# Kernel tuning notes

Hardware: AMD Instinct MI355X
Metric: run time of the kernel (lower is better)

The kernel has to match this reference:

```python
import jax, jax.numpy as jnp
import numpy as np
import math

D = 256; NH = 8; NL = 1; K = 5; P = K * K; HD = D // NH; DFF = 1024
N = 8192; H = 512; W = 512


def _kernel_indices():
    # odd kernel: linspace(-(K-1)/2, (K-1)/2, K) / K, meshgrid ij, stacked (x=j, y=i)
    idx = jnp.linspace(-(K - 1) / 2, (K - 1) / 2, K)
    i, j = jnp.meshgrid(idx, idx, indexing='ij')
    return jnp.stack([j, i], axis=-1).reshape(-1, 2) / K  # (P, 2)


def _ln(x, g, b, eps=1e-5):
    m = x.mean(-1, keepdims=True)
    v = ((x - m) ** 2).mean(-1, keepdims=True)
    return (x - m) / jnp.sqrt(v + eps) * g + b


def setup_inputs() -> dict:
    key = jax.random.key(0)
    ks = jax.random.split(key, 20)
    s = 0.02
    inp = {
        'query': jax.random.normal(ks[0], (1, N, D), jnp.float32),
        'memory': jax.random.normal(ks[1], (1, H * W, D), jnp.float32),
        'ref_windows': jax.random.uniform(ks[2], (1, N, 8), jnp.float32),
        'memory_shape': jnp.array([[H, W]], jnp.int32),
        'memory_start_idx': jnp.zeros((1,), jnp.int64),
        # pos embed MLP(8 -> D -> D -> D)
        'Wp1': jax.random.normal(ks[3], (D, 8)) * s, 'bp1': jnp.zeros((D,)),
        'Wp2': jax.random.normal(ks[4], (D, D)) * s, 'bp2': jnp.zeros((D,)),
        'Wp3': jax.random.normal(ks[5], (D, D)) * s, 'bp3': jnp.zeros((D,)),
        # Box3dAttention
        'Wv': jax.random.normal(ks[6], (D, D)) * s, 'bv': jnp.zeros((D,)),
        'Wa': jax.random.normal(ks[7], (NH * NL * P, D)) * s, 'ba': jnp.zeros((NH * NL * P,)),
        'Wb': jax.random.normal(ks[8], (NH * NL * 5, D)) * s, 'bb': jnp.zeros((NH * NL * 5,)),
        'Wo': jax.random.normal(ks[9], (D, D)) * s, 'bo': jnp.zeros((D,)),
        # FFN + norms
        'W1': jax.random.normal(ks[10], (DFF, D)) * s, 'b1': jnp.zeros((DFF,)),
        'W2': jax.random.normal(ks[11], (D, DFF)) * s, 'b2': jnp.zeros((D,)),
        'g2': jnp.ones((D,)), 'be2': jnp.zeros((D,)),
        'g3': jnp.ones((D,)), 'be3': jnp.zeros((D,)),
    }
    return inp


def reference(query, memory, ref_windows, memory_shape, memory_start_idx,
              Wp1, bp1, Wp2, bp2, Wp3, bp3, Wv, bv, Wa, ba, Wb, bb, Wo, bo,
              W1, b1, W2, b2, g2, be2, g3, be3):
    B, n, _ = query.shape  # B == 1, single level (NL == 1)
    # query positional embedding from ref windows (3-layer MLP)
    qp = jax.nn.relu(ref_windows @ Wp1.T + bp1)
    qp = jax.nn.relu(qp @ Wp2.T + bp2)
    qp = qp @ Wp3.T + bp3
    q = query + qp

    # --- Box3dAttention ---
    v = (memory @ Wv.T + bv).reshape(B, H * W, NH, HD)
    attn = jax.nn.softmax((q @ Wa.T + ba).reshape(B, n, NH, NL * P), axis=-1)
    attn = attn.reshape(B, n, NH, NL, P)

    off = (q @ Wb.T + bb).reshape(B, n, NH, NL, 5)
    off_box, off_ang = off[..., :4], off[..., 4:]
    rw = ref_windows[:, :, None, None]                     # (B,n,1,1,8)
    ref_boxes = rw[..., jnp.array([0, 1, 3, 4])]           # cx,cy,w,l
    ref_angle = rw[..., 6:7]
    angles = (ref_angle + off_ang / 16.0) * (2.0 * math.pi)  # (B,n,NH,NL,1)
    boxes = ref_boxes + off_box / 8.0 * ref_boxes[..., jnp.array([2, 3, 2, 3])]
    center = boxes[..., None, :2]                          # (B,n,NH,NL,1,2)
    size = jax.nn.relu(boxes[..., None, 2:])
    grid = _kernel_indices() * size                        # (B,n,NH,NL,P,2)
    c, sgn = jnp.cos(angles), jnp.sin(angles)
    rot = jnp.stack([c, -sgn, sgn, c], -1).reshape(B, n, NH, NL, 1, 2, 2)
    loc = center + (grid[..., None, :] * rot).sum(-1)      # (B,n,NH,NL,P,2) in [0,1]

    # bilinear sampling (grid_sample, align_corners=False, zero padding), single level
    loc0 = loc[0, :, :, 0]                                 # (n,NH,P,2)
    vh = v[0].transpose(1, 0, 2)                           # (NH,HW,HD)
    x = loc0[..., 0] * W - 0.5
    y = loc0[..., 1] * H - 0.5
    x0 = jnp.floor(x); y0 = jnp.floor(y)
    hidx = jnp.arange(NH)[None, :, None]
    out = jnp.zeros((n, NH, P, HD), v.dtype)
    for dx, dy in ((0, 0), (1, 0), (0, 1), (1, 1)):
        xi = x0 + dx; yi = y0 + dy
        wgt = (1.0 - jnp.abs(x - xi)) * (1.0 - jnp.abs(y - yi))
        valid = (xi >= 0) & (xi <= W - 1) & (yi >= 0) & (yi <= H - 1)
        idx = (jnp.clip(yi, 0, H - 1) * W + jnp.clip(xi, 0, W - 1)).astype(jnp.int32)
        g = vh[hidx, idx]                                  # (n,NH,P,HD)
        out = out + jnp.where(valid, wgt, 0.0)[..., None] * g
    out = (out * attn[0, :, :, 0, :, None]).sum(2)         # (n,NH,HD)
    q2 = out.reshape(1, n, D) @ Wo.T + bo

    # residual + LN + FFN + LN
    xq = _ln(query + q2, g2, be2)
    ff = jax.nn.relu(xq @ W1.T + b1) @ W2.T + b2
    return _ln(xq + ff, g3, be3)
```

## Files before the change

kernel.cpp:

```cpp
#include <hip/hip_runtime.h>
#include <hip/hip_bf16.h>
#include <math.h>

#define NQ 8192
#define DD 256
#define NHD 8
#define HDD 32
#define PP 25
#define HH 512
#define WW 512
#define HWSZ (HH * WW)
#define DFF 1024

typedef __bf16 bf16_t;
typedef bf16_t bf16x8 __attribute__((ext_vector_type(8)));
typedef bf16_t bf16x4 __attribute__((ext_vector_type(4)));
typedef float f32x4 __attribute__((ext_vector_type(4)));

__global__ __launch_bounds__(256, 2) void wv_kernel(
    const float* __restrict__ A, const bf16_t* __restrict__ Wt,
    const float* __restrict__ bias, __hip_bfloat16* __restrict__ V) {
  const int tid = threadIdx.x;
  const int wave = tid >> 6;
  const int lane = tid & 63;
  const int l15 = lane & 15;
  const int quad = lane >> 4;
  const int wslice = wave * 64;
  const int base = blockIdx.x * 256;

  bf16x8 bfr[4][8];
#pragma unroll
  for (int j = 0; j < 4; j++) {
    const bf16_t* wp = Wt + (size_t)(wslice + j * 16 + l15) * 256 + quad * 8;
#pragma unroll
    for (int kt = 0; kt < 8; kt++) bfr[j][kt] = *(const bf16x8*)(wp + kt * 32);
  }
  float bsv[4];
#pragma unroll
  for (int j = 0; j < 4; j++) bsv[j] = bias[wslice + j * 16 + l15];

  for (int c = 0; c < 16; c++) {
    const int m0 = base + c * 16;
    const float* ap = A + (size_t)(m0 + l15) * 256 + quad * 8;
    float4 av[8][2];
#pragma unroll
    for (int kt = 0; kt < 8; kt++) {
      av[kt][0] = *(const float4*)(ap + kt * 32);
      av[kt][1] = *(const float4*)(ap + kt * 32 + 4);
    }
    f32x4 acc[4];
#pragma unroll
    for (int j = 0; j < 4; j++) acc[j] = (f32x4){0.f, 0.f, 0.f, 0.f};
#pragma unroll
    for (int kt = 0; kt < 8; kt++) {
      bf16x8 afr;
      afr[0] = (bf16_t)av[kt][0].x;
      afr[1] = (bf16_t)av[kt][0].y;
      afr[2] = (bf16_t)av[kt][0].z;
      afr[3] = (bf16_t)av[kt][0].w;
      afr[4] = (bf16_t)av[kt][1].x;
      afr[5] = (bf16_t)av[kt][1].y;
      afr[6] = (bf16_t)av[kt][1].z;
      afr[7] = (bf16_t)av[kt][1].w;
#pragma unroll
      for (int j = 0; j < 4; j++)
        acc[j] = __builtin_amdgcn_mfma_f32_16x16x32_bf16(afr, bfr[j][kt],
                                                         acc[j], 0, 0, 0);
    }
#pragma unroll
    for (int j = 0; j < 4; j++) {
      const int col = wslice + j * 16 + l15;
#pragma unroll
      for (int r = 0; r < 4; r++) {
        const int row = m0 + quad * 4 + r;
        V[(size_t)row * DD + col] = __float2bfloat16(acc[j][r] + bsv[j]);
      }
    }
  }
}

template <int RELU, int ADD_RES, int BF16_OUT>
__global__ __launch_bounds__(256) void gemm_mfma(
    const bf16_t* __restrict__ A, const bf16_t* __restrict__ Wt,
    const float* __restrict__ bias, const float* __restrict__ res,
    void* __restrict__ Cout, int M, int N, int K) {
  __shared__ bf16_t As[128][32];
  __shared__ bf16_t Bs[128][32];
  const int tid = threadIdx.x;
  const int bn = blockIdx.x * 128;
  const int bm = blockIdx.y * 128;
  const int wave = tid >> 6;
  const int lane = tid & 63;
  const int l15 = lane & 15;
  const int quad = lane >> 4;
  const int wm = (wave & 1) * 64;
  const int wn = (wave >> 1) * 64;

  f32x4 acc[4][4];
#pragma unroll
  for (int i = 0; i < 4; i++)
#pragma unroll
    for (int j = 0; j < 4; j++) acc[i][j] = (f32x4){0.f, 0.f, 0.f, 0.f};

  const int srow = tid >> 2;
  const int skq = (tid & 3) * 8;

  for (int k0 = 0; k0 < K; k0 += 32) {
#pragma unroll
    for (int c = 0; c < 2; c++) {
      const int row = c * 64 + srow;
      const bf16_t* gp = A + (long)(bm + row) * K + k0 + skq;
      bf16_t* lp = &As[0][0] + (c * 2048 + wave * 512);
      __builtin_amdgcn_global_load_lds(
          (const __attribute__((address_space(1))) void*)gp,
          (__attribute__((address_space(3))) void*)lp, 16, 0, 0);
    }
#pragma unroll
    for (int c = 0; c < 2; c++) {
      const int row = c * 64 + srow;
      int wrow = bn + row;
      if (wrow >= N) wrow = N - 1;
      const bf16_t* gp = Wt + (long)wrow * K + k0 + skq;
      bf16_t* lp = &Bs[0][0] + (c * 2048 + wave * 512);
      __builtin_amdgcn_global_load_lds(
          (const __attribute__((address_space(1))) void*)gp,
          (__attribute__((address_space(3))) void*)lp, 16, 0, 0);
    }
    __syncthreads();
    bf16x8 af[4], bfr[4];
#pragma unroll
    for (int i = 0; i < 4; i++)
      af[i] = *(bf16x8*)&As[wm + i * 16 + l15][quad * 8];
#pragma unroll
    for (int j = 0; j < 4; j++)
      bfr[j] = *(bf16x8*)&Bs[wn + j * 16 + l15][quad * 8];
#pragma unroll
    for (int i = 0; i < 4; i++)
#pragma unroll
      for (int j = 0; j < 4; j++)
        acc[i][j] = __builtin_amdgcn_mfma_f32_16x16x32_bf16(af[i], bfr[j],
                                                            acc[i][j], 0, 0, 0);
    __syncthreads();
  }

  float bsv[4];
#pragma unroll
  for (int j = 0; j < 4; j++) {
    const int n = bn + wn + j * 16 + l15;
    bsv[j] = (n < N) ? bias[n] : 0.f;
  }
#pragma unroll
  for (int i = 0; i < 4; i++) {
#pragma unroll
    for (int r = 0; r < 4; r++) {
      const int m = bm + wm + i * 16 + quad * 4 + r;
#pragma unroll
      for (int j = 0; j < 4; j++) {
        const int n = bn + wn + j * 16 + l15;
        if (n < N) {
          float v = acc[i][j][r] + bsv[j];
          if (ADD_RES) v += res[(long)m * N + n];
          if (RELU) v = fmaxf(v, 0.f);
          if (BF16_OUT)
            ((__hip_bfloat16*)Cout)[(long)m * N + n] = __float2bfloat16(v);
          else
            ((float*)Cout)[(long)m * N + n] = v;
        }
      }
    }
  }
}

struct CastArgs {
  const float* src[8];
  __hip_bfloat16* dst[8];
  int len[8];
};
__global__ __launch_bounds__(256) void cast_weights(CastArgs a) {
  const int seg = blockIdx.y;
  const int base = blockIdx.x * 1024 + threadIdx.x * 4;
  if (base >= a.len[seg]) return;
  const float4 v = *(const float4*)(a.src[seg] + base);
  __hip_bfloat16* d = a.dst[seg] + base;
  d[0] = __float2bfloat16(v.x);
  d[1] = __float2bfloat16(v.y);
  d[2] = __float2bfloat16(v.z);
  d[3] = __float2bfloat16(v.w);
}

__global__ __launch_bounds__(256) void qp1_kernel(
    const float* __restrict__ rw, const float* __restrict__ Wp1,
    const float* __restrict__ bp1, __hip_bfloat16* __restrict__ out) {
  const int m = blockIdx.x;
  const int d = threadIdx.x;
  __shared__ float r[8];
  if (d < 8) r[d] = rw[m * 8 + d];
  __syncthreads();
  float s = bp1[d];
#pragma unroll
  for (int j = 0; j < 8; j++) s += r[j] * Wp1[d * 8 + j];
  out[(long)m * DD + d] = __float2bfloat16(fmaxf(s, 0.f));
}

__global__ __launch_bounds__(256) void attn_loc_kernel(
    const float* __restrict__ logits, const float* __restrict__ offp,
    const float* __restrict__ rw, float* __restrict__ attn,
    float* __restrict__ loc) {
  const int m = blockIdx.x;
  const int t = threadIdx.x;
  __shared__ float sl[200];
  __shared__ float soff[40];
  __shared__ float srw[8];
  if (t < 200) sl[t] = logits[(long)m * 200 + t];
  if (t >= 208 && t < 248) soff[t - 208] = offp[(long)m * 40 + (t - 208)];
  if (t >= 200 && t < 208) srw[t - 200] = rw[(long)m * 8 + (t - 200)];
  __syncthreads();
  if (t < 8) {
    float mx = -1e30f;
    for (int p = 0; p < 25; p++) mx = fmaxf(mx, sl[t * 25 + p]);
    float s = 0.f;
    for (int p = 0; p < 25; p++) s += __expf(sl[t * 25 + p] - mx);
    const float inv = 1.f / s;
    for (int p = 0; p < 25; p++)
      attn[(long)m * 200 + t * 25 + p] = __expf(sl[t * 25 + p] - mx) * inv;
  }
  if (t < 200) {
    const int h = t / 25;
    const int p = t - h * 25;
    const float cx = srw[0], cy = srw[1], w0 = srw[3], h0 = srw[4],
                ra = srw[6];
    const float ob0 = soff[h * 5 + 0], ob1 = soff[h * 5 + 1],
                ob2 = soff[h * 5 + 2], ob3 = soff[h * 5 + 3],
                oa = soff[h * 5 + 4];
    const float ang = (ra + oa * (1.f / 16.f)) * 6.28318530717958647692f;
    const float bx = cx + ob0 * 0.125f * w0;
    const float by = cy + ob1 * 0.125f * h0;
    const float bw = fmaxf(w0 + ob2 * 0.125f * w0, 0.f);
    const float bh = fmaxf(h0 + ob3 * 0.125f * h0, 0.f);
    const float gx = (float)((p % 5) - 2) * 0.2f * bw;
    const float gy = (float)((p / 5) - 2) * 0.2f * bh;
    float sn, cs;
    __sincosf(ang, &sn, &cs);
    loc[((long)m * 200 + t) * 2 + 0] = bx + cs * gx - sn * gy;
    loc[((long)m * 200 + t) * 2 + 1] = by + sn * gx + cs * gy;
  }
}

__global__ __launch_bounds__(256) void sample_kernel(
    const bf16_t* __restrict__ v, const float* __restrict__ attn,
    const float* __restrict__ loc, bf16_t* __restrict__ out) {
  const int m = blockIdx.x;
  const int t = threadIdx.x;
  const int h = t >> 5;
  const int sub = t & 31;
  const int tap = sub >> 3;
  const int ch4 = (sub & 7) * 4;
  const float fdx = (float)(tap & 1);
  const float fdy = (float)(tap >> 1);
  __shared__ float sat[200];
  __shared__ float slc[400];
  if (t < 200) sat[t] = attn[(long)m * 200 + t];
  slc[t] = loc[(long)m * 400 + t];
  if (t < 144) slc[256 + t] = loc[(long)m * 400 + 256 + t];
  __syncthreads();
  float a0 = 0.f, a1 = 0.f, a2 = 0.f, a3 = 0.f;
  const bf16_t* vb = v + h * HDD + ch4;
  for (int p = 0; p < 25; p++) {
    const float lx = slc[(h * 25 + p) * 2 + 0];
    const float ly = slc[(h * 25 + p) * 2 + 1];
    const float aw = sat[h * 25 + p];
    const float x = lx * (float)WW - 0.5f;
    const float y = ly * (float)HH - 0.5f;
    const float x0 = floorf(x);
    const float y0 = floorf(y);
    const float xi = x0 + fdx;
    const float yi = y0 + fdy;
    const float wgt = (1.f - fabsf(x - xi)) * (1.f - fabsf(y - yi));
    const bool valid = (xi >= 0.f) && (xi <= (float)(WW - 1)) &&
                       (yi >= 0.f) && (yi <= (float)(HH - 1));
    const int xc = (int)fminf(fmaxf(xi, 0.f), (float)(WW - 1));
    const int yc = (int)fminf(fmaxf(yi, 0.f), (float)(HH - 1));
    const int idx = yc * WW + xc;
    const bf16x4 g = *(const bf16x4*)(vb + (size_t)idx * DD);
    const float wv = valid ? aw * wgt : 0.f;
    a0 += wv * (float)g[0];
    a1 += wv * (float)g[1];
    a2 += wv * (float)g[2];
    a3 += wv * (float)g[3];
  }
  a0 += __shfl_xor(a0, 8);  a1 += __shfl_xor(a1, 8);
  a2 += __shfl_xor(a2, 8);  a3 += __shfl_xor(a3, 8);
  a0 += __shfl_xor(a0, 16); a1 += __shfl_xor(a1, 16);
  a2 += __shfl_xor(a2, 16); a3 += __shfl_xor(a3, 16);
  if (tap == 0) {
    bf16x4 o;
    o[0] = (bf16_t)a0; o[1] = (bf16_t)a1; o[2] = (bf16_t)a2; o[3] = (bf16_t)a3;
    *(bf16x4*)(out + (size_t)m * DD + h * HDD + ch4) = o;
  }
}

__global__ __launch_bounds__(256) void ln_kernel(
    const float* __restrict__ x, const float* __restrict__ resid,
    const float* __restrict__ g, const float* __restrict__ b,
    float* __restrict__ out, __hip_bfloat16* __restrict__ out_bf) {
  const int m = blockIdx.x;
  const int d = threadIdx.x;
  const float v = x[(long)m * DD + d] + resid[(long)m * DD + d];
  __shared__ float red[256];
  __shared__ float mean_s, inv_s;
  red[d] = v;
  __syncthreads();
  for (int s = 128; s > 0; s >>= 1) {
    if (d < s) red[d] += red[d + s];
    __syncthreads();
  }
  if (d == 0) mean_s = red[0] * (1.f / 256.f);
  __syncthreads();
  const float mu = mean_s;
  const float diff = v - mu;
  red[d] = diff * diff;
  __syncthreads();
  for (int s = 128; s > 0; s >>= 1) {
    if (d < s) red[d] += red[d + s];
    __syncthreads();
  }
  if (d == 0) inv_s = rsqrtf(red[0] * (1.f / 256.f) + 1e-5f);
  __syncthreads();
  const float o = diff * inv_s * g[d] + b[d];
  out[(long)m * DD + d] = o;
  if (out_bf) out_bf[(long)m * DD + d] = __float2bfloat16(o);
}

extern "C" void kernel_launch(void* const* d_in, const int* in_sizes, int n_in,
                              void* d_out, int out_size, void* d_ws,
                              size_t ws_size, hipStream_t stream) {
  const float* query = (const float*)d_in[0];
  const float* memory = (const float*)d_in[1];
  const float* rw = (const float*)d_in[2];
  const float* Wp1 = (const float*)d_in[5];
  const float* bp1 = (const float*)d_in[6];
  const float* Wp2 = (const float*)d_in[7];
  const float* bp2 = (const float*)d_in[8];
  const float* Wp3 = (const float*)d_in[9];
  const float* bp3 = (const float*)d_in[10];
  const float* Wv = (const float*)d_in[11];
  const float* bv = (const float*)d_in[12];
  const float* Wa = (const float*)d_in[13];
  const float* ba = (const float*)d_in[14];
  const float* Wb = (const float*)d_in[15];
  const float* bb = (const float*)d_in[16];
  const float* Wo = (const float*)d_in[17];
  const float* bo = (const float*)d_in[18];
  const float* W1 = (const float*)d_in[19];
  const float* b1 = (const float*)d_in[20];
  const float* W2 = (const float*)d_in[21];
  const float* b2 = (const float*)d_in[22];
  const float* g2 = (const float*)d_in[23];
  const float* be2 = (const float*)d_in[24];
  const float* g3 = (const float*)d_in[25];
  const float* be3 = (const float*)d_in[26];

  char* ws = (char*)d_ws;
  size_t off = 0;
  auto alloc = [&](size_t bytes) {
    void* p = ws + off;
    off += (bytes + 255) & ~(size_t)255;
    return p;
  };
  __hip_bfloat16* vbuf = (__hip_bfloat16*)alloc((size_t)HWSZ * DD * 2);
  __hip_bfloat16* qp1bf = (__hip_bfloat16*)alloc((size_t)NQ * DD * 2);
  __hip_bfloat16* qp2bf = (__hip_bfloat16*)alloc((size_t)NQ * DD * 2);
  __hip_bfloat16* qbf = (__hip_bfloat16*)alloc((size_t)NQ * DD * 2);
  __hip_bfloat16* oabf = (__hip_bfloat16*)alloc((size_t)NQ * DD * 2);
  __hip_bfloat16* xqbf = (__hip_bfloat16*)alloc((size_t)NQ * DD * 2);
  __hip_bfloat16* h1bf = (__hip_bfloat16*)alloc((size_t)NQ * DFF * 2);
  float* xq32 = (float*)alloc((size_t)NQ * DD * 4);
  float* f32buf = (float*)alloc((size_t)NQ * DD * 4);
  float* offbuf = (float*)alloc((size_t)NQ * 40 * 4);
  float* attnbuf = (float*)alloc((size_t)NQ * 200 * 4);
  float* locbuf = (float*)alloc((size_t)NQ * 200 * 2 * 4);
  __hip_bfloat16* Wp2b = (__hip_bfloat16*)alloc(65536 * 2);
  __hip_bfloat16* Wp3b = (__hip_bfloat16*)alloc(65536 * 2);
  __hip_bfloat16* Wvb = (__hip_bfloat16*)alloc(65536 * 2);
  __hip_bfloat16* Wab = (__hip_bfloat16*)alloc(51200 * 2);
  __hip_bfloat16* Wbb = (__hip_bfloat16*)alloc(10240 * 2);
  __hip_bfloat16* Wob = (__hip_bfloat16*)alloc(65536 * 2);
  __hip_bfloat16* W1b = (__hip_bfloat16*)alloc(262144 * 2);
  __hip_bfloat16* W2b = (__hip_bfloat16*)alloc(262144 * 2);
  (void)ws_size;

  CastArgs ca;
  ca.src[0] = Wp2; ca.dst[0] = Wp2b; ca.len[0] = 65536;
  ca.src[1] = Wp3; ca.dst[1] = Wp3b; ca.len[1] = 65536;
  ca.src[2] = Wv;  ca.dst[2] = Wvb;  ca.len[2] = 65536;
  ca.src[3] = Wa;  ca.dst[3] = Wab;  ca.len[3] = 51200;
  ca.src[4] = Wb;  ca.dst[4] = Wbb;  ca.len[4] = 10240;
  ca.src[5] = Wo;  ca.dst[5] = Wob;  ca.len[5] = 65536;
  ca.src[6] = W1;  ca.dst[6] = W1b;  ca.len[6] = 262144;
  ca.src[7] = W2;  ca.dst[7] = W2b;  ca.len[7] = 262144;
  cast_weights<<<dim3(256, 8), 256, 0, stream>>>(ca);

  qp1_kernel<<<NQ, 256, 0, stream>>>(rw, Wp1, bp1, qp1bf);
  gemm_mfma<1, 0, 1><<<dim3(2, NQ / 128), 256, 0, stream>>>(
      (const bf16_t*)qp1bf, (const bf16_t*)Wp2b, bp2, nullptr, qp2bf, NQ, DD,
      DD);
  gemm_mfma<0, 1, 1><<<dim3(2, NQ / 128), 256, 0, stream>>>(
      (const bf16_t*)qp2bf, (const bf16_t*)Wp3b, bp3, query, qbf, NQ, DD, DD);
  wv_kernel<<<HWSZ / 256, 256, 0, stream>>>(memory, (const bf16_t*)Wvb, bv,
                                            vbuf);
  gemm_mfma<0, 0, 0><<<dim3(2, NQ / 128), 256, 0, stream>>>(
      (const bf16_t*)qbf, (const bf16_t*)Wab, ba, nullptr, f32buf, NQ, 200,
      DD);
  gemm_mfma<0, 0, 0><<<dim3(1, NQ / 128), 256, 0, stream>>>(
      (const bf16_t*)qbf, (const bf16_t*)Wbb, bb, nullptr, offbuf, NQ, 40, DD);
  attn_loc_kernel<<<NQ, 256, 0, stream>>>(f32buf, offbuf, rw, attnbuf, locbuf);
  sample_kernel<<<NQ, 256, 0, stream>>>((const bf16_t*)vbuf, attnbuf, locbuf,
                                        (bf16_t*)oabf);
  gemm_mfma<0, 0, 0><<<dim3(2, NQ / 128), 256, 0, stream>>>(
      (const bf16_t*)oabf, (const bf16_t*)Wob, bo, nullptr, f32buf, NQ, DD,
      DD);
  ln_kernel<<<NQ, 256, 0, stream>>>(f32buf, query, g2, be2, xq32, xqbf);
  gemm_mfma<1, 0, 1><<<dim3(8, NQ / 128), 256, 0, stream>>>(
      (const bf16_t*)xqbf, (const bf16_t*)W1b, b1, nullptr, h1bf, NQ, DFF, DD);
  gemm_mfma<0, 0, 0><<<dim3(2, NQ / 128), 256, 0, stream>>>(
      (const bf16_t*)h1bf, (const bf16_t*)W2b, b2, nullptr, f32buf, NQ, DD,
      DFF);
  ln_kernel<<<NQ, 256, 0, stream>>>(f32buf, xq32, g3, be3, (float*)d_out,
                                    nullptr);
}
```

Measured before the change: 825.6 us.

## Retile memory value projection, merge attn/offset GEMMs, fuse softmax+loc into sampler

The value projection over the 262144-row memory is retiled. Each block now stages a 64-column slice of the weights in shared memory, computes a 256x64 output tile with 4x4 MFMA accumulators per wave, and writes bf16x4 vector stores instead of scalar ones. The attention-logit and box-offset GEMMs are merged into one 240-column GEMM by using a split bias. The softmax and sampling-location computation moves into the sampling kernel, which removes a kernel launch and the attn/loc buffer round trips. In exchange, each block in the value projection rereads the fp32 memory rows four times, once per column slice, and the sampling kernel gains an extra barrier.

```diff
diff --git a/kernel.cpp b/kernel.cpp
--- a/kernel.cpp
+++ b/kernel.cpp
@@ -17,64 +17,72 @@
 typedef bf16_t bf16x4 __attribute__((ext_vector_type(4)));
 typedef float f32x4 __attribute__((ext_vector_type(4)));
 
-__global__ __launch_bounds__(256, 2) void wv_kernel(
+__global__ __launch_bounds__(256) void wv_kernel(
     const float* __restrict__ A, const bf16_t* __restrict__ Wt,
-    const float* __restrict__ bias, __hip_bfloat16* __restrict__ V) {
+    const float* __restrict__ bias, bf16_t* __restrict__ V) {
+  __shared__ bf16_t Bs[64][264];
   const int tid = threadIdx.x;
   const int wave = tid >> 6;
   const int lane = tid & 63;
   const int l15 = lane & 15;
   const int quad = lane >> 4;
-  const int wslice = wave * 64;
-  const int base = blockIdx.x * 256;
-
-  bf16x8 bfr[4][8];
-#pragma unroll
-  for (int j = 0; j < 4; j++) {
-    const bf16_t* wp = Wt + (size_t)(wslice + j * 16 + l15) * 256 + quad * 8;
-#pragma unroll
-    for (int kt = 0; kt < 8; kt++) bfr[j][kt] = *(const bf16x8*)(wp + kt * 32);
-  }
+  const int nbase = (blockIdx.x & 3) * 64;
+  const int mbase = (blockIdx.x >> 2) * 256;
+
+  {
+    const int rr = tid & 63;
+    const int seg = tid >> 6;
+    const int wrow = nbase + ((rr & 15) * 4 + (rr >> 4));
+    const bf16_t* gp = Wt + (size_t)wrow * 256 + seg * 64;
+#pragma unroll
+    for (int u = 0; u < 8; u++)
+      *(bf16x8*)&Bs[rr][seg * 64 + u * 8] = *(const bf16x8*)(gp + u * 8);
+  }
+  __syncthreads();
+
+  const int m0 = mbase + wave * 64;
+  f32x4 acc[4][4];
+#pragma unroll
+  for (int i = 0; i < 4; i++)
+#pragma unroll
+    for (int j = 0; j < 4; j++) acc[i][j] = (f32x4){0.f, 0.f, 0.f, 0.f};
   float bsv[4];
 #pragma unroll
-  for (int j = 0; j < 4; j++) bsv[j] = bias[wslice + j * 16 + l15];
-
-  for (int c = 0; c < 16; c++) {
-    const int m0 = base + c * 16;
-    const float* ap = A + (size_t)(m0 + l15) * 256 + quad * 8;
-    float4 av[8][2];
-#pragma unroll
-    for (int kt = 0; kt < 8; kt++) {
-      av[kt][0] = *(const float4*)(ap + kt * 32);
-      av[kt][1] = *(const float4*)(ap + kt * 32 + 4);
-    }
-    f32x4 acc[4];
-#pragma unroll
-    for (int j = 0; j < 4; j++) acc[j] = (f32x4){0.f, 0.f, 0.f, 0.f};
-#pragma unroll
-    for (int kt = 0; kt < 8; kt++) {
-      bf16x8 afr;
-      afr[0] = (bf16_t)av[kt][0].x;
-      afr[1] = (bf16_t)av[kt][0].y;
-      afr[2] = (bf16_t)av[kt][0].z;
-      afr[3] = (bf16_t)av[kt][0].w;
-      afr[4] = (bf16_t)av[kt][1].x;
-      afr[5] = (bf16_t)av[kt][1].y;
-      afr[6] = (bf16_t)av[kt][1].z;
-      afr[7] = (bf16_t)av[kt][1].w;
-#pragma unroll
-      for (int j = 0; j < 4; j++)
-        acc[j] = __builtin_amdgcn_mfma_f32_16x16x32_bf16(afr, bfr[j][kt],
-                                                         acc[j], 0, 0, 0);
+  for (int j = 0; j < 4; j++) bsv[j] = bias[nbase + l15 * 4 + j];
+
+#pragma unroll
+  for (int kt = 0; kt < 8; kt++) {
+    const int k0 = kt * 32;
+    bf16x8 afr[4];
+#pragma unroll
+    for (int i = 0; i < 4; i++) {
+      const float* ap = A + (size_t)(m0 + i * 16 + l15) * 256 + k0 + quad * 8;
+      const float4 a0 = *(const float4*)ap;
+      const float4 a1 = *(const float4*)(ap + 4);
+      afr[i][0] = (bf16_t)a0.x; afr[i][1] = (bf16_t)a0.y;
+      afr[i][2] = (bf16_t)a0.z; afr[i][3] = (bf16_t)a0.w;
+      afr[i][4] = (bf16_t)a1.x; afr[i][5] = (bf16_t)a1.y;
+      afr[i][6] = (bf16_t)a1.z; afr[i][7] = (bf16_t)a1.w;
     }
 #pragma unroll
     for (int j = 0; j < 4; j++) {
-      const int col = wslice + j * 16 + l15;
-#pragma unroll
-      for (int r = 0; r < 4; r++) {
-        const int row = m0 + quad * 4 + r;
-        V[(size_t)row * DD + col] = __float2bfloat16(acc[j][r] + bsv[j]);
-      }
+      const bf16x8 bfr = *(const bf16x8*)&Bs[j * 16 + l15][k0 + quad * 8];
+#pragma unroll
+      for (int i = 0; i < 4; i++)
+        acc[i][j] = __builtin_amdgcn_mfma_f32_16x16x32_bf16(afr[i], bfr,
+                                                            acc[i][j], 0, 0, 0);
+    }
+  }
+
+#pragma unroll
+  for (int i = 0; i < 4; i++) {
+#pragma unroll
+    for (int r = 0; r < 4; r++) {
+      const int row = m0 + i * 16 + quad * 4 + r;
+      bf16x4 o;
+#pragma unroll
+      for (int j = 0; j < 4; j++) o[j] = (bf16_t)(acc[i][j][r] + bsv[j]);
+      *(bf16x4*)(V + (size_t)row * DD + nbase + l15 * 4) = o;
     }
   }
 }
@@ -82,8 +90,9 @@
 template <int RELU, int ADD_RES, int BF16_OUT>
 __global__ __launch_bounds__(256) void gemm_mfma(
     const bf16_t* __restrict__ A, const bf16_t* __restrict__ Wt,
-    const float* __restrict__ bias, const float* __restrict__ res,
-    void* __restrict__ Cout, int M, int N, int K) {
+    const float* __restrict__ bias, const float* __restrict__ bias2, int split,
+    const float* __restrict__ res, void* __restrict__ Cout, int M, int N,
+    int K) {
   __shared__ bf16_t As[128][32];
   __shared__ bf16_t Bs[128][32];
   const int tid = threadIdx.x;
@@ -147,7 +156,7 @@
 #pragma unroll
   for (int j = 0; j < 4; j++) {
     const int n = bn + wn + j * 16 + l15;
-    bsv[j] = (n < N) ? bias[n] : 0.f;
+    bsv[j] = (n >= N) ? 0.f : (n < split ? bias[n] : bias2[n - split]);
   }
 #pragma unroll
   for (int i = 0; i < 4; i++) {
@@ -202,53 +211,9 @@
   out[(long)m * DD + d] = __float2bfloat16(fmaxf(s, 0.f));
 }
 
-__global__ __launch_bounds__(256) void attn_loc_kernel(
-    const float* __restrict__ logits, const float* __restrict__ offp,
-    const float* __restrict__ rw, float* __restrict__ attn,
-    float* __restrict__ loc) {
-  const int m = blockIdx.x;
-  const int t = threadIdx.x;
-  __shared__ float sl[200];
-  __shared__ float soff[40];
-  __shared__ float srw[8];
-  if (t < 200) sl[t] = logits[(long)m * 200 + t];
-  if (t >= 208 && t < 248) soff[t - 208] = offp[(long)m * 40 + (t - 208)];
-  if (t >= 200 && t < 208) srw[t - 200] = rw[(long)m * 8 + (t - 200)];
-  __syncthreads();
-  if (t < 8) {
-    float mx = -1e30f;
-    for (int p = 0; p < 25; p++) mx = fmaxf(mx, sl[t * 25 + p]);
-    float s = 0.f;
-    for (int p = 0; p < 25; p++) s += __expf(sl[t * 25 + p] - mx);
-    const float inv = 1.f / s;
-    for (int p = 0; p < 25; p++)
-      attn[(long)m * 200 + t * 25 + p] = __expf(sl[t * 25 + p] - mx) * inv;
-  }
-  if (t < 200) {
-    const int h = t / 25;
-    const int p = t - h * 25;
-    const float cx = srw[0], cy = srw[1], w0 = srw[3], h0 = srw[4],
-                ra = srw[6];
-    const float ob0 = soff[h * 5 + 0], ob1 = soff[h * 5 + 1],
-                ob2 = soff[h * 5 + 2], ob3 = soff[h * 5 + 3],
-                oa = soff[h * 5 + 4];
-    const float ang = (ra + oa * (1.f / 16.f)) * 6.28318530717958647692f;
-    const float bx = cx + ob0 * 0.125f * w0;
-    const float by = cy + ob1 * 0.125f * h0;
-    const float bw = fmaxf(w0 + ob2 * 0.125f * w0, 0.f);
-    const float bh = fmaxf(h0 + ob3 * 0.125f * h0, 0.f);
-    const float gx = (float)((p % 5) - 2) * 0.2f * bw;
-    const float gy = (float)((p / 5) - 2) * 0.2f * bh;
-    float sn, cs;
-    __sincosf(ang, &sn, &cs);
-    loc[((long)m * 200 + t) * 2 + 0] = bx + cs * gx - sn * gy;
-    loc[((long)m * 200 + t) * 2 + 1] = by + sn * gx + cs * gy;
-  }
-}
-
 __global__ __launch_bounds__(256) void sample_kernel(
-    const bf16_t* __restrict__ v, const float* __restrict__ attn,
-    const float* __restrict__ loc, bf16_t* __restrict__ out) {
+    const bf16_t* __restrict__ v, const float* __restrict__ lg,
+    const float* __restrict__ rw, bf16_t* __restrict__ out) {
   const int m = blockIdx.x;
   const int t = threadIdx.x;
   const int h = t >> 5;
@@ -257,11 +222,40 @@
   const int ch4 = (sub & 7) * 4;
   const float fdx = (float)(tap & 1);
   const float fdy = (float)(tap >> 1);
+  __shared__ float sl[240];
+  __shared__ float srw[8];
   __shared__ float sat[200];
   __shared__ float slc[400];
-  if (t < 200) sat[t] = attn[(long)m * 200 + t];
-  slc[t] = loc[(long)m * 400 + t];
-  if (t < 144) slc[256 + t] = loc[(long)m * 400 + 256 + t];
+  if (t < 240) sl[t] = lg[(long)m * 240 + t];
+  if (t >= 240 && t < 248) srw[t - 240] = rw[(long)m * 8 + (t - 240)];
+  __syncthreads();
+  if (t < 8) {
+    float mx = -1e30f;
+    for (int p = 0; p < 25; p++) mx = fmaxf(mx, sl[t * 25 + p]);
+    float s = 0.f;
+    for (int p = 0; p < 25; p++) s += __expf(sl[t * 25 + p] - mx);
+    const float inv = 1.f / s;
+    for (int p = 0; p < 25; p++)
+      sat[t * 25 + p] = __expf(sl[t * 25 + p] - mx) * inv;
+  }
+  if (t < 200) {
+    const int hh = t / 25;
+    const int p = t - hh * 25;
+    const float cx = srw[0], cy = srw[1], w0 = srw[3], h0 = srw[4],
+                ra = srw[6];
+    const float* o5 = &sl[200 + hh * 5];
+    const float ang = (ra + o5[4] * (1.f / 16.f)) * 6.28318530717958647692f;
+    const float bx = cx + o5[0] * 0.125f * w0;
+    const float by = cy + o5[1] * 0.125f * h0;
+    const float bw = fmaxf(w0 + o5[2] * 0.125f * w0, 0.f);
+    const float bh = fmaxf(h0 + o5[3] * 0.125f * h0, 0.f);
+    const float gx = (float)((p % 5) - 2) * 0.2f * bw;
+    const float gy = (float)((p / 5) - 2) * 0.2f * bh;
+    float sn, cs;
+    __sincosf(ang, &sn, &cs);
+    slc[t * 2 + 0] = bx + cs * gx - sn * gy;
+    slc[t * 2 + 1] = by + sn * gx + cs * gy;
+  }
   __syncthreads();
   float a0 = 0.f, a1 = 0.f, a2 = 0.f, a3 = 0.f;
   const bf16_t* vb = v + h * HDD + ch4;
@@ -376,55 +370,51 @@
   __hip_bfloat16* h1bf = (__hip_bfloat16*)alloc((size_t)NQ * DFF * 2);
   float* xq32 = (float*)alloc((size_t)NQ * DD * 4);
   float* f32buf = (float*)alloc((size_t)NQ * DD * 4);
-  float* offbuf = (float*)alloc((size_t)NQ * 40 * 4);
-  float* attnbuf = (float*)alloc((size_t)NQ * 200 * 4);
-  float* locbuf = (float*)alloc((size_t)NQ * 200 * 2 * 4);
+  float* lgbuf = (float*)alloc((size_t)NQ * 240 * 4);
   __hip_bfloat16* Wp2b = (__hip_bfloat16*)alloc(65536 * 2);
   __hip_bfloat16* Wp3b = (__hip_bfloat16*)alloc(65536 * 2);
   __hip_bfloat16* Wvb = (__hip_bfloat16*)alloc(65536 * 2);
-  __hip_bfloat16* Wab = (__hip_bfloat16*)alloc(51200 * 2);
-  __hip_bfloat16* Wbb = (__hip_bfloat16*)alloc(10240 * 2);
+  __hip_bfloat16* Wabb = (__hip_bfloat16*)alloc(61440 * 2);
   __hip_bfloat16* Wob = (__hip_bfloat16*)alloc(65536 * 2);
   __hip_bfloat16* W1b = (__hip_bfloat16*)alloc(262144 * 2);
   __hip_bfloat16* W2b = (__hip_bfloat16*)alloc(262144 * 2);
   (void)ws_size;
 
   CastArgs ca;
-  ca.src[0] = Wp2; ca.dst[0] = Wp2b; ca.len[0] = 65536;
-  ca.src[1] = Wp3; ca.dst[1] = Wp3b; ca.len[1] = 65536;
-  ca.src[2] = Wv;  ca.dst[2] = Wvb;  ca.len[2] = 65536;
-  ca.src[3] = Wa;  ca.dst[3] = Wab;  ca.len[3] = 51200;
-  ca.src[4] = Wb;  ca.dst[4] = Wbb;  ca.len[4] = 10240;
-  ca.src[5] = Wo;  ca.dst[5] = Wob;  ca.len[5] = 65536;
-  ca.src[6] = W1;  ca.dst[6] = W1b;  ca.len[6] = 262144;
-  ca.src[7] = W2;  ca.dst[7] = W2b;  ca.len[7] = 262144;
+  ca.src[0] = Wp2; ca.dst[0] = Wp2b;          ca.len[0] = 65536;
+  ca.src[1] = Wp3; ca.dst[1] = Wp3b;          ca.len[1] = 65536;
+  ca.src[2] = Wv;  ca.dst[2] = Wvb;           ca.len[2] = 65536;
+  ca.src[3] = Wa;  ca.dst[3] = Wabb;          ca.len[3] = 51200;
+  ca.src[4] = Wb;  ca.dst[4] = Wabb + 51200;  ca.len[4] = 10240;
+  ca.src[5] = Wo;  ca.dst[5] = Wob;           ca.len[5] = 65536;
+  ca.src[6] = W1;  ca.dst[6] = W1b;           ca.len[6] = 262144;
+  ca.src[7] = W2;  ca.dst[7] = W2b;           ca.len[7] = 262144;
   cast_weights<<<dim3(256, 8), 256, 0, stream>>>(ca);
 
   qp1_kernel<<<NQ, 256, 0, stream>>>(rw, Wp1, bp1, qp1bf);
   gemm_mfma<1, 0, 1><<<dim3(2, NQ / 128), 256, 0, stream>>>(
-      (const bf16_t*)qp1bf, (const bf16_t*)Wp2b, bp2, nullptr, qp2bf, NQ, DD,
-      DD);
+      (const bf16_t*)qp1bf, (const bf16_t*)Wp2b, bp2, nullptr, 1 << 30,
+      nullptr, qp2bf, NQ, DD, DD);
   gemm_mfma<0, 1, 1><<<dim3(2, NQ / 128), 256, 0, stream>>>(
-      (const bf16_t*)qp2bf, (const bf16_t*)Wp3b, bp3, query, qbf, NQ, DD, DD);
-  wv_kernel<<<HWSZ / 256, 256, 0, stream>>>(memory, (const bf16_t*)Wvb, bv,
-                                            vbuf);
+      (const bf16_t*)qp2bf, (const bf16_t*)Wp3b, bp3, nullptr, 1 << 30, query,
+      qbf, NQ, DD, DD);
+  wv_kernel<<<(HWSZ / 256) * 4, 256, 0, stream>>>(memory, (const bf16_t*)Wvb,
+                                                  bv, (bf16_t*)vbuf);
   gemm_mfma<0, 0, 0><<<dim3(2, NQ / 128), 256, 0, stream>>>(
-      (const bf16_t*)qbf, (const bf16_t*)Wab, ba, nullptr, f32buf, NQ, 200,
-      DD);
-  gemm_mfma<0, 0, 0><<<dim3(1, NQ / 128), 256, 0, stream>>>(
-      (const bf16_t*)qbf, (const bf16_t*)Wbb, bb, nullptr, offbuf, NQ, 40, DD);
-  attn_loc_kernel<<<NQ, 256, 0, stream>>>(f32buf, offbuf, rw, attnbuf, locbuf);
-  sample_kernel<<<NQ, 256, 0, stream>>>((const bf16_t*)vbuf, attnbuf, locbuf,
+      (const bf16_t*)qbf, (const bf16_t*)Wabb, ba, bb, 200, nullptr, lgbuf,
+      NQ, 240, DD);
+  sample_kernel<<<NQ, 256, 0, stream>>>((const bf16_t*)vbuf, lgbuf, rw,
                                         (bf16_t*)oabf);
   gemm_mfma<0, 0, 0><<<dim3(2, NQ / 128), 256, 0, stream>>>(
-      (const bf16_t*)oabf, (const bf16_t*)Wob, bo, nullptr, f32buf, NQ, DD,
-      DD);
+      (const bf16_t*)oabf, (const bf16_t*)Wob, bo, nullptr, 1 << 30, nullptr,
+      f32buf, NQ, DD, DD);
   ln_kernel<<<NQ, 256, 0, stream>>>(f32buf, query, g2, be2, xq32, xqbf);
   gemm_mfma<1, 0, 1><<<dim3(8, NQ / 128), 256, 0, stream>>>(
-      (const bf16_t*)xqbf, (const bf16_t*)W1b, b1, nullptr, h1bf, NQ, DFF, DD);
+      (const bf16_t*)xqbf, (const bf16_t*)W1b, b1, nullptr, 1 << 30, nullptr,
+      h1bf, NQ, DFF, DD);
   gemm_mfma<0, 0, 0><<<dim3(2, NQ / 128), 256, 0, stream>>>(
-      (const bf16_t*)h1bf, (const bf16_t*)W2b, b2, nullptr, f32buf, NQ, DD,
-      DFF);
+      (const bf16_t*)h1bf, (const bf16_t*)W2b, b2, nullptr, 1 << 30, nullptr,
+      f32buf, NQ, DD, DFF);
   ln_kernel<<<NQ, 256, 0, stream>>>(f32buf, xq32, g3, be3, (float*)d_out,
                                     nullptr);
 }
```

After: 770.6 us. 1.07x faster.
